# Kernel tuning notes

Hardware: AMD Instinct MI355X
Metric: run time of the kernel (lower is better)

## Reference

```python
import jax, jax.numpy as jnp
import numpy as np

N = 50000          # nodes
E = 600000         # edges (before self-loops)
IN = 256           # input feature dim
HID = 64           # hidden channels per head
HEADS = 4          # attention heads (hidden layers)
OUT = 64           # output channels (last layer, heads=1)
NEG_SLOPE = 0.2    # PyG GATConv default leaky-relu slope


def setup_inputs() -> dict:
    key = jax.random.key(0)
    ks = jax.random.split(key, 16)
    s = 0.05
    x = jax.random.normal(ks[0], (N, IN), jnp.float32)
    edge_index = jax.random.randint(ks[1], (2, E), 0, N, jnp.int32)
    # layer 0: IN -> HEADS*HID
    W0 = jax.random.normal(ks[2], (IN, HEADS * HID), jnp.float32) * s
    a0s = jax.random.normal(ks[3], (HEADS, HID), jnp.float32) * s
    a0d = jax.random.normal(ks[4], (HEADS, HID), jnp.float32) * s
    b0 = jnp.zeros((HEADS * HID,), jnp.float32)
    # layer 1: HEADS*HID -> HEADS*HID
    W1 = jax.random.normal(ks[5], (HEADS * HID, HEADS * HID), jnp.float32) * s
    a1s = jax.random.normal(ks[6], (HEADS, HID), jnp.float32) * s
    a1d = jax.random.normal(ks[7], (HEADS, HID), jnp.float32) * s
    b1 = jnp.zeros((HEADS * HID,), jnp.float32)
    # layer 2 (output): HEADS*HID -> OUT, heads=1
    W2 = jax.random.normal(ks[8], (HEADS * HID, OUT), jnp.float32) * s
    a2s = jax.random.normal(ks[9], (1, OUT), jnp.float32) * s
    a2d = jax.random.normal(ks[10], (1, OUT), jnp.float32) * s
    b2 = jnp.zeros((OUT,), jnp.float32)
    return dict(x=x, edge_index=edge_index,
                W0=W0, a0s=a0s, a0d=a0d, b0=b0,
                W1=W1, a1s=a1s, a1d=a1d, b1=b1,
                W2=W2, a2s=a2s, a2d=a2d, b2=b2)


def _gat_conv(x, src, dst, deg, W, a_s, a_d, b, heads, out_ch):
    """PyG-style GATConv with self-loops already in (src, dst); mean aggregation."""
    n = x.shape[0]
    h = (x @ W).reshape(n, heads, out_ch)                 # [N, H, C]
    alpha_s = jnp.sum(h * a_s, axis=-1)                   # [N, H]
    alpha_d = jnp.sum(h * a_d, axis=-1)                   # [N, H]
    e = jax.nn.leaky_relu(alpha_s[src] + alpha_d[dst], NEG_SLOPE)  # [Etot, H]
    # segment softmax over incoming edges of each dst node
    m = jax.ops.segment_max(e, dst, num_segments=n)       # [N, H]
    ex = jnp.exp(e - m[dst])
    denom = jax.ops.segment_sum(ex, dst, num_segments=n)  # [N, H]
    alpha = ex / denom[dst]                               # [Etot, H]
    msg = h[src] * alpha[..., None]                       # [Etot, H, C]
    out = jax.ops.segment_sum(msg, dst, num_segments=n)   # [N, H, C]
    out = out / deg[:, None, None]                        # aggr='mean'
    return out.reshape(n, heads * out_ch) + b


def reference(x, edge_index, W0, a0s, a0d, b0, W1, a1s, a1d, b1, W2, a2s, a2d, b2):
    n = x.shape[0]
    # PyG GATConv adds self-loops by default; edge_index constant across layers
    loop = jnp.arange(n, dtype=edge_index.dtype)
    src = jnp.concatenate([edge_index[0], loop])
    dst = jnp.concatenate([edge_index[1], loop])
    deg = jax.ops.segment_sum(jnp.ones(src.shape[0], jnp.float32), dst, num_segments=n)
    h = _gat_conv(x, src, dst, deg, W0, a0s, a0d, b0, HEADS, HID)
    h = jax.nn.relu(h)   # dropout is identity at inference
    h = _gat_conv(h, src, dst, deg, W1, a1s, a1d, b1, HEADS, HID)
    h = jax.nn.relu(h)
    out = _gat_conv(h, src, dst, deg, W2, a2s, a2d, b2, 1, OUT)
    return out
```

## Files before the change

### kernel.cpp

```cpp
#include <hip/hip_runtime.h>
#include <hip/hip_fp16.h>

#define NEG_SLOPE 0.2f

typedef _Float16 f16x8 __attribute__((ext_vector_type(8)));
typedef _Float16 f16x4 __attribute__((ext_vector_type(4)));
typedef float f32x4 __attribute__((ext_vector_type(4)));

__global__ void zero_int_kernel(int* __restrict__ p, int n) {
  int i = blockIdx.x * blockDim.x + threadIdx.x;
  if (i < n) p[i] = 0;
}

__global__ void count_kernel(const int* __restrict__ ei, int E, int N,
                             int* __restrict__ cnt) {
  int e = blockIdx.x * blockDim.x + threadIdx.x;
  int tot = E + N;
  if (e >= tot) return;
  int dst = (e < E) ? ei[E + e] : (e - E);
  atomicAdd(&cnt[dst], 1);
}

__global__ __launch_bounds__(1024) void scan_kernel(const int* __restrict__ cnt,
                                                    int* __restrict__ row_ptr,
                                                    int* __restrict__ cursor,
                                                    int N) {
  int t = threadIdx.x;
  int CH = (N + 1023) >> 10;
  int b = t * CH; if (b > N) b = N;
  int e = b + CH; if (e > N) e = N;
  int sum = 0;
  for (int i = b; i < e; ++i) sum += cnt[i];
  int lane = t & 63, wid = t >> 6;
  int v = sum;
#pragma unroll
  for (int off = 1; off < 64; off <<= 1) {
    int u = __shfl_up(v, off, 64);
    if (lane >= off) v += u;
  }
  __shared__ int wsum[16];
  __shared__ int wpre[16];
  if (lane == 63) wsum[wid] = v;
  __syncthreads();
  if (t < 16) {
    int wv = wsum[t];
#pragma unroll
    for (int off = 1; off < 16; off <<= 1) {
      int u = __shfl_up(wv, off, 16);
      if (t >= off) wv += u;
    }
    wpre[t] = wv - wsum[t];
  }
  __syncthreads();
  int run = wpre[wid] + (v - sum);
  for (int i = b; i < e; ++i) {
    int c = cnt[i];
    row_ptr[i] = run;
    cursor[i] = run;
    run += c;
  }
  if (t == 1023) row_ptr[N] = run;
}

__global__ void fill_kernel(const int* __restrict__ ei, int E, int N,
                            int* __restrict__ cursor, int* __restrict__ col_src) {
  int e = blockIdx.x * blockDim.x + threadIdx.x;
  int tot = E + N;
  if (e >= tot) return;
  int src, dst;
  if (e < E) { src = ei[e]; dst = ei[E + e]; } else { src = e - E; dst = e - E; }
  int pos = atomicAdd(&cursor[dst], 1);
  col_src[pos] = src;
}

template <int BN>
__global__ __launch_bounds__(256) void mfma_gemm(const float* __restrict__ X,
                                                 const float* __restrict__ W,
                                                 float* __restrict__ Y,
                                                 __half* __restrict__ Y16,
                                                 int M, int N, int K) {
  constexpr int BM = 128, BK = 32;
  constexpr int LDK = BK + 8;
  constexpr int MI = (BN == 128) ? 4 : 2;
  constexpr int NI = 4;
  constexpr int CK = BN / 8;
  __shared__ _Float16 Ah[BM][LDK];
  __shared__ _Float16 Al[BM][LDK];
  __shared__ _Float16 Bh[BN][LDK];
  __shared__ _Float16 Bl[BN][LDK];
  int tid = threadIdx.x;
  int wave = tid >> 6, lane = tid & 63;
  int quad = lane >> 4, l16 = lane & 15;
  int br = blockIdx.y * BM, bc = blockIdx.x * BN;
  int wm = (BN == 128) ? (wave >> 1) * 64 : wave * 32;
  int wn = (BN == 128) ? (wave & 1) * 64 : 0;
  int bn = tid % BN;
  int bkh = (tid / BN) * CK;

  f32x4 acc[MI][NI] = {};

  for (int k0 = 0; k0 < K; k0 += BK) {
#pragma unroll
    for (int i = 0; i < 4; ++i) {
      int f = tid + i * 256;
      int row = f >> 3;
      int kq = (f & 7) * 4;
      int gm = br + row;
      float4 v = make_float4(0.f, 0.f, 0.f, 0.f);
      if (gm < M) v = *(const float4*)&X[(size_t)gm * K + k0 + kq];
      f16x4 hi, lo;
      hi[0] = (_Float16)v.x; lo[0] = (_Float16)(v.x - (float)hi[0]);
      hi[1] = (_Float16)v.y; lo[1] = (_Float16)(v.y - (float)hi[1]);
      hi[2] = (_Float16)v.z; lo[2] = (_Float16)(v.z - (float)hi[2]);
      hi[3] = (_Float16)v.w; lo[3] = (_Float16)(v.w - (float)hi[3]);
      *(f16x4*)&Ah[row][kq] = hi;
      *(f16x4*)&Al[row][kq] = lo;
    }
    {
      float tmp[CK];
#pragma unroll
      for (int i = 0; i < CK; ++i)
        tmp[i] = W[(size_t)(k0 + bkh + i) * N + bc + bn];
#pragma unroll
      for (int c = 0; c < CK / 8; ++c) {
        f16x8 hi8, lo8;
#pragma unroll
        for (int j = 0; j < 8; ++j) {
          float v = tmp[c * 8 + j];
          _Float16 h = (_Float16)v;
          hi8[j] = h;
          lo8[j] = (_Float16)(v - (float)h);
        }
        *(f16x8*)&Bh[bn][bkh + c * 8] = hi8;
        *(f16x8*)&Bl[bn][bkh + c * 8] = lo8;
      }
    }
    __syncthreads();
    f16x8 fah[MI], fal[MI], fbh[NI], fbl[NI];
#pragma unroll
    for (int mi = 0; mi < MI; ++mi) {
      int row = wm + mi * 16 + l16;
      fah[mi] = *(const f16x8*)&Ah[row][quad * 8];
      fal[mi] = *(const f16x8*)&Al[row][quad * 8];
    }
#pragma unroll
    for (int ni = 0; ni < NI; ++ni) {
      int col = wn + ni * 16 + l16;
      fbh[ni] = *(const f16x8*)&Bh[col][quad * 8];
      fbl[ni] = *(const f16x8*)&Bl[col][quad * 8];
    }
#pragma unroll
    for (int mi = 0; mi < MI; ++mi)
#pragma unroll
      for (int ni = 0; ni < NI; ++ni) {
        acc[mi][ni] = __builtin_amdgcn_mfma_f32_16x16x32_f16(
            fah[mi], fbh[ni], acc[mi][ni], 0, 0, 0);
        acc[mi][ni] = __builtin_amdgcn_mfma_f32_16x16x32_f16(
            fah[mi], fbl[ni], acc[mi][ni], 0, 0, 0);
        acc[mi][ni] = __builtin_amdgcn_mfma_f32_16x16x32_f16(
            fal[mi], fbh[ni], acc[mi][ni], 0, 0, 0);
      }
    __syncthreads();
  }

#pragma unroll
  for (int mi = 0; mi < MI; ++mi) {
#pragma unroll
    for (int r = 0; r < 4; ++r) {
      int grow = br + wm + mi * 16 + quad * 4 + r;
      if (grow >= M) continue;
#pragma unroll
      for (int ni = 0; ni < NI; ++ni) {
        int gcol = bc + wn + ni * 16 + l16;
        float v = acc[mi][ni][r];
        Y[(size_t)grow * N + gcol] = v;
        Y16[(size_t)grow * N + gcol] = __float2half(v);
      }
    }
  }
}

template <int H, int C>
__global__ void alpha_kernel(const float* __restrict__ h,
                             const float* __restrict__ a_s,
                             const float* __restrict__ a_d,
                             float* __restrict__ out_s,
                             float* __restrict__ out_d, int N) {
  constexpr int HC = H * C;
  constexpr int PER = HC / 64;
  constexpr int SEG = C / PER;
  int lane = threadIdx.x & 63;
  int node = (blockIdx.x * blockDim.x + threadIdx.x) >> 6;
  if (node >= N) return;
  int cbase = lane * PER;
  const float* row = h + (size_t)node * HC + cbase;
  float ss, dd;
  if constexpr (PER == 4) {
    float4 v = *(const float4*)row;
    float4 s4 = *(const float4*)(a_s + cbase);
    float4 d4 = *(const float4*)(a_d + cbase);
    ss = v.x * s4.x + v.y * s4.y + v.z * s4.z + v.w * s4.w;
    dd = v.x * d4.x + v.y * d4.y + v.z * d4.z + v.w * d4.w;
  } else {
    float v = row[0];
    ss = v * a_s[cbase];
    dd = v * a_d[cbase];
  }
#pragma unroll
  for (int off = SEG >> 1; off >= 1; off >>= 1) {
    ss += __shfl_xor(ss, off, 64);
    dd += __shfl_xor(dd, off, 64);
  }
  if ((lane % SEG) == 0) {
    int head = lane / SEG;
    out_s[(size_t)node * H + head] = ss;
    out_d[(size_t)node * H + head] = dd;
  }
}

__device__ __forceinline__ void fma_h4(const __half* p, float w, float* facc) {
  union { float2 f2; __half2 h2[2]; } c;
  c.f2 = *(const float2*)p;
  float2 lo = __half22float2(c.h2[0]);
  float2 hi = __half22float2(c.h2[1]);
  facc[0] += lo.x * w; facc[1] += lo.y * w;
  facc[2] += hi.x * w; facc[3] += hi.y * w;
}

template <bool RELU>
__global__ void aggregate4_kernel(const __half* __restrict__ h16,
                                  const float* __restrict__ as_,
                                  const float* __restrict__ ad_,
                                  const int* __restrict__ row_ptr,
                                  const int* __restrict__ col_src,
                                  const float* __restrict__ bias,
                                  float* __restrict__ out, int N) {
  int lane = threadIdx.x & 63;
  int node = (blockIdx.x * blockDim.x + threadIdx.x) >> 6;
  if (node >= N) return;
  int beg = row_ptr[node], end = row_ptr[node + 1];
  int deg = end - beg;
  float inv_deg = 1.f / (float)deg;
  int myhead = lane >> 4;
  float facc[4] = {};
  float4 adv4 = *(const float4*)(ad_ + (size_t)node * 4);
  const __half* hl = h16 + lane * 4;

  if (deg <= 16) {
    int head_w = lane >> 4, e_w = lane & 15;
    float q = 0.f; int s_w = 0;
    if (e_w < deg) {
      s_w = col_src[beg + e_w];
      float4 a4 = *(const float4*)(as_ + (size_t)s_w * 4);
      float av = head_w == 0 ? a4.x : head_w == 1 ? a4.y : head_w == 2 ? a4.z : a4.w;
      float dv = head_w == 0 ? adv4.x : head_w == 1 ? adv4.y : head_w == 2 ? adv4.z : adv4.w;
      float e = av + dv;
      e = (e > 0.f) ? e : NEG_SLOPE * e;
      q = __expf(e);
    }
    float dn = q;
    dn += __shfl_xor(dn, 1, 64);
    dn += __shfl_xor(dn, 2, 64);
    dn += __shfl_xor(dn, 4, 64);
    dn += __shfl_xor(dn, 8, 64);
    float qs = q * (1.f / dn) * inv_deg;
    int base = myhead << 4;
    int i = 0;
    for (; i + 4 <= deg; i += 4) {
      int s0 = __shfl(s_w, base + i + 0, 64); float w0 = __shfl(qs, base + i + 0, 64);
      int s1 = __shfl(s_w, base + i + 1, 64); float w1 = __shfl(qs, base + i + 1, 64);
      int s2 = __shfl(s_w, base + i + 2, 64); float w2 = __shfl(qs, base + i + 2, 64);
      int s3 = __shfl(s_w, base + i + 3, 64); float w3 = __shfl(qs, base + i + 3, 64);
      fma_h4(hl + (size_t)s0 * 256, w0, facc);
      fma_h4(hl + (size_t)s1 * 256, w1, facc);
      fma_h4(hl + (size_t)s2 * 256, w2, facc);
      fma_h4(hl + (size_t)s3 * 256, w3, facc);
    }
    for (; i < deg; ++i) {
      int srcn = __shfl(s_w, base + i, 64);
      float w = __shfl(qs, base + i, 64);
      fma_h4(hl + (size_t)srcn * 256, w, facc);
    }
  } else if (deg <= 64) {
    float p0 = 0.f, p1 = 0.f, p2 = 0.f, p3 = 0.f; int s_w = 0;
    if (lane < deg) {
      s_w = col_src[beg + lane];
      float4 a4 = *(const float4*)(as_ + (size_t)s_w * 4);
      float e0 = a4.x + adv4.x; e0 = e0 > 0.f ? e0 : NEG_SLOPE * e0; p0 = __expf(e0);
      float e1 = a4.y + adv4.y; e1 = e1 > 0.f ? e1 : NEG_SLOPE * e1; p1 = __expf(e1);
      float e2 = a4.z + adv4.z; e2 = e2 > 0.f ? e2 : NEG_SLOPE * e2; p2 = __expf(e2);
      float e3 = a4.w + adv4.w; e3 = e3 > 0.f ? e3 : NEG_SLOPE * e3; p3 = __expf(e3);
    }
    float d0 = p0, d1 = p1, d2 = p2, d3 = p3;
#pragma unroll
    for (int off = 32; off >= 1; off >>= 1) {
      d0 += __shfl_xor(d0, off, 64);
      d1 += __shfl_xor(d1, off, 64);
      d2 += __shfl_xor(d2, off, 64);
      d3 += __shfl_xor(d3, off, 64);
    }
    p0 *= (1.f / d0) * inv_deg;
    p1 *= (1.f / d1) * inv_deg;
    p2 *= (1.f / d2) * inv_deg;
    p3 *= (1.f / d3) * inv_deg;
    int i = 0;
    for (; i + 2 <= deg; i += 2) {
      int s0 = __shfl(s_w, i + 0, 64);
      int s1 = __shfl(s_w, i + 1, 64);
      float a00 = __shfl(p0, i + 0, 64), a01 = __shfl(p1, i + 0, 64);
      float a02 = __shfl(p2, i + 0, 64), a03 = __shfl(p3, i + 0, 64);
      float a10 = __shfl(p0, i + 1, 64), a11 = __shfl(p1, i + 1, 64);
      float a12 = __shfl(p2, i + 1, 64), a13 = __shfl(p3, i + 1, 64);
      float w0 = myhead == 0 ? a00 : myhead == 1 ? a01 : myhead == 2 ? a02 : a03;
      float w1 = myhead == 0 ? a10 : myhead == 1 ? a11 : myhead == 2 ? a12 : a13;
      fma_h4(hl + (size_t)s0 * 256, w0, facc);
      fma_h4(hl + (size_t)s1 * 256, w1, facc);
    }
    for (; i < deg; ++i) {
      int srcn = __shfl(s_w, i, 64);
      float b0 = __shfl(p0, i, 64), b1 = __shfl(p1, i, 64);
      float b2 = __shfl(p2, i, 64), b3 = __shfl(p3, i, 64);
      float w = myhead == 0 ? b0 : myhead == 1 ? b1 : myhead == 2 ? b2 : b3;
      fma_h4(hl + (size_t)srcn * 256, w, facc);
    }
  } else {
    float dn0 = 0.f, dn1 = 0.f, dn2 = 0.f, dn3 = 0.f;
    for (int i = beg + lane; i < end; i += 64) {
      int s = col_src[i];
      float4 a4 = *(const float4*)(as_ + (size_t)s * 4);
      float e0 = a4.x + adv4.x; e0 = e0 > 0.f ? e0 : NEG_SLOPE * e0; dn0 += __expf(e0);
      float e1 = a4.y + adv4.y; e1 = e1 > 0.f ? e1 : NEG_SLOPE * e1; dn1 += __expf(e1);
      float e2 = a4.z + adv4.z; e2 = e2 > 0.f ? e2 : NEG_SLOPE * e2; dn2 += __expf(e2);
      float e3 = a4.w + adv4.w; e3 = e3 > 0.f ? e3 : NEG_SLOPE * e3; dn3 += __expf(e3);
    }
#pragma unroll
    for (int off = 32; off >= 1; off >>= 1) {
      dn0 += __shfl_xor(dn0, off, 64);
      dn1 += __shfl_xor(dn1, off, 64);
      dn2 += __shfl_xor(dn2, off, 64);
      dn3 += __shfl_xor(dn3, off, 64);
    }
    float adm = myhead == 0 ? adv4.x : myhead == 1 ? adv4.y : myhead == 2 ? adv4.z : adv4.w;
    float invdn = 1.f / (myhead == 0 ? dn0 : myhead == 1 ? dn1 : myhead == 2 ? dn2 : dn3);
    invdn *= inv_deg;
    for (int i = beg; i < end; ++i) {
      int s = col_src[i];
      float e = as_[(size_t)s * 4 + myhead] + adm;
      e = (e > 0.f) ? e : NEG_SLOPE * e;
      float w = __expf(e) * invdn;
      fma_h4(hl + (size_t)s * 256, w, facc);
    }
  }

  float* orow = out + (size_t)node * 256 + lane * 4;
#pragma unroll
  for (int p = 0; p < 4; ++p) {
    float v = facc[p] + bias[lane * 4 + p];
    if (RELU) v = fmaxf(v, 0.f);
    orow[p] = v;
  }
}

template <bool RELU>
__global__ void aggregate1_kernel(const __half* __restrict__ h16,
                                  const float* __restrict__ as_,
                                  const float* __restrict__ ad_,
                                  const int* __restrict__ row_ptr,
                                  const int* __restrict__ col_src,
                                  const float* __restrict__ bias,
                                  float* __restrict__ out, int N) {
  int lane = threadIdx.x & 63;
  int node = (blockIdx.x * blockDim.x + threadIdx.x) >> 6;
  if (node >= N) return;
  int beg = row_ptr[node], end = row_ptr[node + 1];
  int deg = end - beg;
  float inv_deg = 1.f / (float)deg;
  float adv = ad_[node];
  const __half* hb = h16 + lane;
  float facc = 0.f;

  if (deg <= 64) {
    float q = 0.f; int s_w = 0;
    if (lane < deg) {
      s_w = col_src[beg + lane];
      float e = as_[s_w] + adv;
      e = (e > 0.f) ? e : NEG_SLOPE * e;
      q = __expf(e);
    }
    float dn = q;
#pragma unroll
    for (int off = 32; off >= 1; off >>= 1) dn += __shfl_xor(dn, off, 64);
    float qs = q * (1.f / dn) * inv_deg;
    int deg8 = (deg + 7) & ~7;
    for (int i = 0; i < deg8; i += 8) {
      int s0 = __shfl(s_w, i + 0, 64); float w0 = __shfl(qs, i + 0, 64);
      int s1 = __shfl(s_w, i + 1, 64); float w1 = __shfl(qs, i + 1, 64);
      int s2 = __shfl(s_w, i + 2, 64); float w2 = __shfl(qs, i + 2, 64);
      int s3 = __shfl(s_w, i + 3, 64); float w3 = __shfl(qs, i + 3, 64);
      int s4 = __shfl(s_w, i + 4, 64); float w4 = __shfl(qs, i + 4, 64);
      int s5 = __shfl(s_w, i + 5, 64); float w5 = __shfl(qs, i + 5, 64);
      int s6 = __shfl(s_w, i + 6, 64); float w6 = __shfl(qs, i + 6, 64);
      int s7 = __shfl(s_w, i + 7, 64); float w7 = __shfl(qs, i + 7, 64);
      float v0 = __half2float(hb[(size_t)s0 * 64]);
      float v1 = __half2float(hb[(size_t)s1 * 64]);
      float v2 = __half2float(hb[(size_t)s2 * 64]);
      float v3 = __half2float(hb[(size_t)s3 * 64]);
      float v4 = __half2float(hb[(size_t)s4 * 64]);
      float v5 = __half2float(hb[(size_t)s5 * 64]);
      float v6 = __half2float(hb[(size_t)s6 * 64]);
      float v7 = __half2float(hb[(size_t)s7 * 64]);
      facc += v0 * w0 + v1 * w1 + v2 * w2 + v3 * w3;
      facc += v4 * w4 + v5 * w5 + v6 * w6 + v7 * w7;
    }
  } else {
    float dn = 0.f;
    for (int i = beg + lane; i < end; i += 64) {
      int s = col_src[i];
      float e = as_[s] + adv;
      e = (e > 0.f) ? e : NEG_SLOPE * e;
      dn += __expf(e);
    }
#pragma unroll
    for (int off = 32; off >= 1; off >>= 1) dn += __shfl_xor(dn, off, 64);
    float scale = (1.f / dn) * inv_deg;
    for (int base = beg; base < end; base += 64) {
      int i2 = base + lane;
      float q2 = 0.f; int s2r = 0;
      if (i2 < end) {
        s2r = col_src[i2];
        float e = as_[s2r] + adv;
        e = (e > 0.f) ? e : NEG_SLOPE * e;
        q2 = __expf(e) * scale;
      }
      int cnt = end - base; if (cnt > 64) cnt = 64;
      for (int j = 0; j < cnt; ++j) {
        int s = __shfl(s2r, j, 64);
        float w = __shfl(q2, j, 64);
        facc += __half2float(hb[(size_t)s * 64]) * w;
      }
    }
  }

  float vout = facc + bias[lane];
  if (RELU) vout = fmaxf(vout, 0.f);
  out[(size_t)node * 64 + lane] = vout;
}

extern "C" void kernel_launch(void* const* d_in, const int* in_sizes, int n_in,
                              void* d_out, int out_size, void* d_ws, size_t ws_size,
                              hipStream_t stream) {
  const float* x   = (const float*)d_in[0];
  const int*   ei  = (const int*)d_in[1];
  const float* W0  = (const float*)d_in[2];
  const float* a0s = (const float*)d_in[3];
  const float* a0d = (const float*)d_in[4];
  const float* b0  = (const float*)d_in[5];
  const float* W1  = (const float*)d_in[6];
  const float* a1s = (const float*)d_in[7];
  const float* a1d = (const float*)d_in[8];
  const float* b1  = (const float*)d_in[9];
  const float* W2  = (const float*)d_in[10];
  const float* a2s = (const float*)d_in[11];
  const float* a2d = (const float*)d_in[12];
  const float* b2  = (const float*)d_in[13];

  const int IN = 256;
  const int N = in_sizes[0] / IN;
  const int E = in_sizes[1] / 2;
  const int Etot = E + N;

  char* ws = (char*)d_ws;
  size_t off = 0;
  auto alloc = [&](size_t bytes) {
    void* p = ws + off;
    off += (bytes + 255) & ~(size_t)255;
    return p;
  };
  float*  A       = (float*)alloc((size_t)N * 256 * 4);
  float*  Bbuf    = (float*)alloc((size_t)N * 256 * 4);
  __half* A16     = (__half*)alloc((size_t)N * 256 * 2);
  float*  as_buf  = (float*)alloc((size_t)N * 4 * 4);
  float*  ad_buf  = (float*)alloc((size_t)N * 4 * 4);
  int*    row_ptr = (int*)alloc((size_t)(N + 1) * 4);
  int*    cursor  = (int*)alloc((size_t)N * 4);
  int*    cnt     = (int*)alloc((size_t)N * 4);
  int*    col_src = (int*)alloc((size_t)Etot * 4);

  zero_int_kernel<<<(N + 255) / 256, 256, 0, stream>>>(cnt, N);
  count_kernel<<<(Etot + 255) / 256, 256, 0, stream>>>(ei, E, N, cnt);
  scan_kernel<<<1, 1024, 0, stream>>>(cnt, row_ptr, cursor, N);
  fill_kernel<<<(Etot + 255) / 256, 256, 0, stream>>>(ei, E, N, cursor, col_src);

  dim3 g0(256 / 128, (N + 127) / 128);
  dim3 g2(64 / 64, (N + 127) / 128);
  int node_blocks = (N + 3) / 4;

  mfma_gemm<128><<<g0, 256, 0, stream>>>(x, W0, A, A16, N, 256, 256);
  alpha_kernel<4, 64><<<node_blocks, 256, 0, stream>>>(A, a0s, a0d, as_buf, ad_buf, N);
  aggregate4_kernel<true><<<node_blocks, 256, 0, stream>>>(
      A16, as_buf, ad_buf, row_ptr, col_src, b0, Bbuf, N);

  mfma_gemm<128><<<g0, 256, 0, stream>>>(Bbuf, W1, A, A16, N, 256, 256);
  alpha_kernel<4, 64><<<node_blocks, 256, 0, stream>>>(A, a1s, a1d, as_buf, ad_buf, N);
  aggregate4_kernel<true><<<node_blocks, 256, 0, stream>>>(
      A16, as_buf, ad_buf, row_ptr, col_src, b1, Bbuf, N);

  mfma_gemm<64><<<g2, 256, 0, stream>>>(Bbuf, W2, A, A16, N, 64, 256);
  alpha_kernel<1, 64><<<node_blocks, 256, 0, stream>>>(A, a2s, a2d, as_buf, ad_buf, N);
  aggregate1_kernel<false><<<node_blocks, 256, 0, stream>>>(
      A16, as_buf, ad_buf, row_ptr, col_src, b2, (float*)d_out, N);
}
```

Before: 565.4 us.

## Replace single-block prefix scan with three-phase multi-block scan

The exclusive scan over per-node edge counts used to run in one 1024-thread block, with each thread walking a strided chunk of about 49 elements serially. It is now split into three kernels: a per-1024-element block scan with vectorized int4 loads, a single-wavefront scan of the block totals, and an elementwise pass that adds the block offsets and writes row_ptr and cursor. This spreads the scan across many CUs and gives coalesced access, at the cost of two extra kernel launches and an intermediate buffer.

```diff
diff --git a/kernel.cpp b/kernel.cpp
--- a/kernel.cpp
+++ b/kernel.cpp
@@ -21,45 +21,81 @@
   atomicAdd(&cnt[dst], 1);
 }
 
-__global__ __launch_bounds__(1024) void scan_kernel(const int* __restrict__ cnt,
-                                                    int* __restrict__ row_ptr,
-                                                    int* __restrict__ cursor,
+__global__ __launch_bounds__(256) void scanA_kernel(const int* __restrict__ cnt,
+                                                    int* __restrict__ locex,
+                                                    int* __restrict__ blk_sum,
                                                     int N) {
   int t = threadIdx.x;
-  int CH = (N + 1023) >> 10;
-  int b = t * CH; if (b > N) b = N;
-  int e = b + CH; if (e > N) e = N;
-  int sum = 0;
-  for (int i = b; i < e; ++i) sum += cnt[i];
+  int base = blockIdx.x * 1024 + t * 4;
+  int a0 = 0, a1 = 0, a2 = 0, a3 = 0;
+  if (base + 3 < N) {
+    int4 v = *(const int4*)&cnt[base];
+    a0 = v.x; a1 = v.y; a2 = v.z; a3 = v.w;
+  } else if (base < N) {
+    a0 = cnt[base];
+    if (base + 1 < N) a1 = cnt[base + 1];
+    if (base + 2 < N) a2 = cnt[base + 2];
+  }
+  int s1 = a0 + a1, s2 = s1 + a2, s3 = s2 + a3;
+  int tot = s3;
   int lane = t & 63, wid = t >> 6;
-  int v = sum;
+  int ws = tot;
 #pragma unroll
   for (int off = 1; off < 64; off <<= 1) {
-    int u = __shfl_up(v, off, 64);
-    if (lane >= off) v += u;
-  }
-  __shared__ int wsum[16];
-  __shared__ int wpre[16];
-  if (lane == 63) wsum[wid] = v;
+    int u = __shfl_up(ws, off, 64);
+    if (lane >= off) ws += u;
+  }
+  __shared__ int wsum[4];
+  __shared__ int woff[4];
+  if (lane == 63) wsum[wid] = ws;
   __syncthreads();
-  if (t < 16) {
-    int wv = wsum[t];
-#pragma unroll
-    for (int off = 1; off < 16; off <<= 1) {
-      int u = __shfl_up(wv, off, 16);
-      if (t >= off) wv += u;
-    }
-    wpre[t] = wv - wsum[t];
+  if (t == 0) {
+    int r = 0;
+#pragma unroll
+    for (int i = 0; i < 4; ++i) { woff[i] = r; r += wsum[i]; }
+    blk_sum[blockIdx.x] = r;
   }
   __syncthreads();
-  int run = wpre[wid] + (v - sum);
-  for (int i = b; i < e; ++i) {
-    int c = cnt[i];
-    row_ptr[i] = run;
-    cursor[i] = run;
-    run += c;
-  }
-  if (t == 1023) row_ptr[N] = run;
+  int ex = woff[wid] + (ws - tot);
+  int o0 = ex, o1 = ex + a0, o2 = ex + s1, o3 = ex + s2;
+  if (base + 3 < N) {
+    *(int4*)&locex[base] = make_int4(o0, o1, o2, o3);
+  } else if (base < N) {
+    locex[base] = o0;
+    if (base + 1 < N) locex[base + 1] = o1;
+    if (base + 2 < N) locex[base + 2] = o2;
+  }
+}
+
+__global__ void scanB_kernel(const int* __restrict__ blk_sum,
+                             int* __restrict__ blk_off,
+                             int* __restrict__ row_ptr, int nb, int N) {
+  int t = threadIdx.x;
+  int run = 0;
+  for (int c = 0; c < nb; c += 64) {
+    int idx = c + t;
+    int v = (idx < nb) ? blk_sum[idx] : 0;
+    int inc = v;
+#pragma unroll
+    for (int off = 1; off < 64; off <<= 1) {
+      int u = __shfl_up(inc, off, 64);
+      if (t >= off) inc += u;
+    }
+    if (idx < nb) blk_off[idx] = run + inc - v;
+    run += __shfl(inc, 63, 64);
+  }
+  if (t == 0) row_ptr[N] = run;
+}
+
+__global__ void scanC_kernel(const int* __restrict__ locex,
+                             const int* __restrict__ blk_off,
+                             int* __restrict__ row_ptr,
+                             int* __restrict__ cursor, int N) {
+  int i = blockIdx.x * blockDim.x + threadIdx.x;
+  if (i >= N) return;
+  int v = blk_off[i >> 10] + locex[i];
+  row_ptr[i] = v;
+  cursor[i] = v;
 }
 
 __global__ void fill_kernel(const int* __restrict__ ei, int E, int N,
@@ -468,6 +504,7 @@
   const int N = in_sizes[0] / IN;
   const int E = in_sizes[1] / 2;
   const int Etot = E + N;
+  const int nb = (N + 1023) / 1024;
 
   char* ws = (char*)d_ws;
   size_t off = 0;
@@ -485,10 +522,15 @@
   int*    cursor  = (int*)alloc((size_t)N * 4);
   int*    cnt     = (int*)alloc((size_t)N * 4);
   int*    col_src = (int*)alloc((size_t)Etot * 4);
+  int*    locex   = (int*)alloc((size_t)N * 4);
+  int*    blk_sum = (int*)alloc((size_t)nb * 4);
+  int*    blk_off = (int*)alloc((size_t)nb * 4);
 
   zero_int_kernel<<<(N + 255) / 256, 256, 0, stream>>>(cnt, N);
   count_kernel<<<(Etot + 255) / 256, 256, 0, stream>>>(ei, E, N, cnt);
-  scan_kernel<<<1, 1024, 0, stream>>>(cnt, row_ptr, cursor, N);
+  scanA_kernel<<<nb, 256, 0, stream>>>(cnt, locex, blk_sum, N);
+  scanB_kernel<<<1, 64, 0, stream>>>(blk_sum, blk_off, row_ptr, nb, N);
+  scanC_kernel<<<(N + 255) / 256, 256, 0, stream>>>(locex, blk_off, row_ptr, cursor, N);
   fill_kernel<<<(Etot + 255) / 256, 256, 0, stream>>>(ei, E, N, cursor, col_src);
 
   dim3 g0(256 / 128, (N + 127) / 128);
```

New measurement: 461.0 us. -18.5%, faster.
